# Performance work log

Measured on AMD Instinct MI355X. Metric: run time of the kernel, lower is better.

Reference implementation:

```python
import jax, jax.numpy as jnp
import numpy as np

H = 16
D_NOPE = 128
D_ROPE = 64
D_V = 128
ROPE_BASE = 10000.0
NEG = -1e9


def rotate_half(x):
    h = x.shape[-1] // 2
    return jnp.concatenate([-x[..., h:], x[..., :h]], axis=-1)


def rope_cos_sin(L, dtype=jnp.float32):
    inv_freq = 1.0 / (ROPE_BASE ** (jnp.arange(0, D_ROPE, 2, dtype=jnp.float32) / D_ROPE))
    t = jnp.arange(L, dtype=jnp.float32)
    freqs = jnp.outer(t, inv_freq)                      # (L, D_ROPE/2)
    emb = jnp.concatenate([freqs, freqs], axis=-1)      # (L, D_ROPE)
    return jnp.cos(emb)[None, None].astype(dtype), jnp.sin(emb)[None, None].astype(dtype)


def setup_inputs() -> dict:
    key = jax.random.key(0)
    ks = jax.random.split(key, 8)
    B, L, D = 1, 2048, 2048
    dq, dc = 1536, 512
    dqk = D_NOPE + D_ROPE
    s = 0.02
    hidden_states = jax.random.normal(ks[0], (B, L, D), jnp.float32)
    # causal additive mask, shape (B,1,L,L)
    causal = jnp.tril(jnp.ones((L, L), jnp.bool_))
    attention_mask = jnp.where(causal, 0.0, NEG).astype(jnp.float32)[None, None]
    return {
        "hidden_states": hidden_states,
        "attention_mask": attention_mask,
        "Wq_down": jax.random.normal(ks[1], (D, dq), jnp.float32) * s,
        "Wq_up": jax.random.normal(ks[2], (dq, H * dqk), jnp.float32) * s,
        "Wkv_down": jax.random.normal(ks[3], (D, dc), jnp.float32) * s,
        "Wk_up": jax.random.normal(ks[4], (dc, H * dqk), jnp.float32) * s,
        "Wv_up": jax.random.normal(ks[5], (dc, H * D_V), jnp.float32) * s,
        "Wo": jax.random.normal(ks[6], (H * D_V, D), jnp.float32) * s,
    }


def reference(hidden_states, attention_mask, Wq_down, Wq_up, Wkv_down, Wk_up, Wv_up, Wo):
    B, L, D = hidden_states.shape
    dqk = D_NOPE + D_ROPE
    scale = 1.0 / np.sqrt(dqk).astype(np.float32)

    # low-rank Q path
    q = (hidden_states @ Wq_down) @ Wq_up                       # (B,L,H*dqk)
    q = q.reshape(B, L, H, dqk).transpose(0, 2, 1, 3)           # (B,H,L,dqk)
    # low-rank KV path
    c_kv = hidden_states @ Wkv_down                             # (B,L,dc)
    k = (c_kv @ Wk_up).reshape(B, L, H, dqk).transpose(0, 2, 1, 3)
    v = (c_kv @ Wv_up).reshape(B, L, H, D_V).transpose(0, 2, 1, 3)

    q_nope, q_rope = q[..., :D_NOPE], q[..., D_NOPE:]
    k_nope, k_rope = k[..., :D_NOPE], k[..., D_NOPE:]
    cos, sin = rope_cos_sin(L, hidden_states.dtype)
    q_rope = q_rope * cos + rotate_half(q_rope) * sin
    k_rope = k_rope * cos + rotate_half(k_rope) * sin
    q = jnp.concatenate([q_nope, q_rope], axis=-1)
    k = jnp.concatenate([k_nope, k_rope], axis=-1)

    scores = jnp.einsum("bhqd,bhkd->bhqk", q, k) * scale + attention_mask
    weights = jax.nn.softmax(scores.astype(jnp.float32), axis=-1).astype(q.dtype)
    attn = jnp.einsum("bhqk,bhkd->bhqd", weights, v)            # (B,H,L,D_V)
    attn = attn.transpose(0, 2, 1, 3).reshape(B, L, H * D_V)
    return attn @ Wo
```

## Files before the change

kernel.cpp:

```cpp
#include <hip/hip_runtime.h>
#include <hip/hip_bf16.h>

using bf16 = __hip_bfloat16;
typedef __bf16 bf16x8v __attribute__((ext_vector_type(8)));
typedef float f32x4 __attribute__((ext_vector_type(4)));

static constexpr int SEQ = 2048;
static constexpr int DMODEL = 2048;
static constexpr int NHEADS = 16;
static constexpr int DQKC = 192;
static constexpr int DVC = 128;
static constexpr int DQC = 1536;
static constexpr int DCC = 512;
static constexpr int HQK = NHEADS * DQKC;
static constexpr int HV = NHEADS * DVC;
static constexpr int NKV = HQK + HV;
static constexpr int NDOWN = DQC + DCC;

typedef __attribute__((address_space(1))) const void* gas_ptr;
typedef __attribute__((address_space(3))) void* las_ptr;

__device__ __forceinline__ void g2l16(const void* g, void* l) {
  __builtin_amdgcn_global_load_lds((gas_ptr)g, (las_ptr)l, 16, 0, 0);
}

__global__ __launch_bounds__(256) void gemm_bt(
    const bf16* __restrict__ A, int lda, long strideAz,
    const bf16* __restrict__ Bt, int ldb, long strideBz,
    void* __restrict__ Cv, int ldc, long strideCz,
    int K, float alpha, int c_fp32, int causal)
{
  if (causal == 1 && blockIdx.x > blockIdx.y) return;
  int Keff = K;
  if (causal == 2) Keff = min(K, ((int)blockIdx.y + 1) * 128);
  __shared__ __align__(16) bf16 As[128 * 32];
  __shared__ __align__(16) bf16 Bs[128 * 32];
  const int z = blockIdx.z;
  A += (long)z * strideAz;
  Bt += (long)z * strideBz;
  const int tid = threadIdx.x;
  const int wv = tid >> 6;
  const int lane = tid & 63;
  const int wm = (wv >> 1) * 64, wn = (wv & 1) * 64;
  const long tm = (long)blockIdx.y * 128, tn = (long)blockIdx.x * 128;
  const int r16 = lane >> 2;
  const int c8 = (lane & 3) * 8;
  const bf16* Ag = A + (tm + wv * 32 + r16) * lda + c8;
  const bf16* Bg = Bt + (tn + wv * 32 + r16) * ldb + c8;
  bf16* lA0 = &As[(wv * 32) * 32];
  bf16* lA1 = &As[(wv * 32 + 16) * 32];
  bf16* lB0 = &Bs[(wv * 32) * 32];
  bf16* lB1 = &Bs[(wv * 32 + 16) * 32];
  const int m0 = lane & 15;
  const int q8 = (lane >> 4) * 8;
  f32x4 acc[4][4] = {};
  for (int bk = 0; bk < Keff; bk += 32) {
    g2l16(Ag + bk, lA0);
    g2l16(Ag + bk + 16 * (long)lda, lA1);
    g2l16(Bg + bk, lB0);
    g2l16(Bg + bk + 16 * (long)ldb, lB1);
    __syncthreads();
    bf16x8v af[4], bfv[4];
#pragma unroll
    for (int i = 0; i < 4; i++)
      af[i] = *reinterpret_cast<const bf16x8v*>(&As[(wm + i * 16 + m0) * 32 + q8]);
#pragma unroll
    for (int i = 0; i < 4; i++)
      bfv[i] = *reinterpret_cast<const bf16x8v*>(&Bs[(wn + i * 16 + m0) * 32 + q8]);
#pragma unroll
    for (int mi = 0; mi < 4; mi++)
#pragma unroll
      for (int ni = 0; ni < 4; ni++)
        acc[mi][ni] = __builtin_amdgcn_mfma_f32_16x16x32_bf16(af[mi], bfv[ni], acc[mi][ni], 0, 0, 0);
    __syncthreads();
  }
  const int q4 = (lane >> 4) * 4;
  float* Cf = (float*)Cv;
  bf16* Cb = (bf16*)Cv;
  const long zc = (long)z * strideCz;
#pragma unroll
  for (int mi = 0; mi < 4; mi++) {
#pragma unroll
    for (int r = 0; r < 4; r++) {
      const long row = tm + wm + mi * 16 + q4 + r;
#pragma unroll
      for (int ni = 0; ni < 4; ni++) {
        const long idx = zc + row * ldc + tn + wn + ni * 16 + m0;
        const float v = acc[mi][ni][r] * alpha;
        if (c_fp32) Cf[idx] = v;
        else Cb[idx] = __float2bfloat16(v);
      }
    }
  }
}

__global__ __launch_bounds__(256) void flash_attn(
    const bf16* __restrict__ qf,
    const bf16* __restrict__ kvf,
    const bf16* __restrict__ vT,
    bf16* __restrict__ attn)
{
  __shared__ __align__(16) char smem[81920];
  const int fid = blockIdx.x;
  const int half = fid >> 8;
  const int r8 = fid & 255;
  const int h = r8 & 15;
  const int t8 = r8 >> 4;
  const int tile = half ? (31 - t8) : t8;
  const int nkt = (tile >> 1) + 1;
  const int tid = threadIdx.x;
  const int w = tid >> 6, lane = tid & 63;
  const int m0 = lane & 15, quad = lane >> 4;
  const int prow = w * 16 + m0;
  const long qrow = (long)tile * 64 + prow;

  bf16x8v qfr[6];
#pragma unroll
  for (int s = 0; s < 6; s++)
    qfr[s] = *reinterpret_cast<const bf16x8v*>(
        &qf[qrow * HQK + h * DQKC + s * 32 + quad * 8]);

  f32x4 O[8] = {};
  float mrow = -1e30f, lrow = 0.f;

  for (int kt = 0; kt < nkt; ++kt) {
    const int key0 = kt * 128;
#pragma unroll
    for (int i = 0; i < 12; i++) {
      const int u = i * 256 + tid;
      const int key = u / 24;
      const int fg = (u - key * 24) ^ (key & 7);
      g2l16(kvf + (long)(key0 + key) * NKV + h * DQKC + fg * 8, smem + u * 16);
    }
#pragma unroll
    for (int i = 0; i < 8; i++) {
      const int u = i * 256 + tid;
      const int dv = u >> 4;
      const int kg = (u & 15) ^ (dv & 15);
      g2l16(vT + (long)(h * DVC + dv) * SEQ + key0 + kg * 8, smem + 49152 + u * 16);
    }
    __syncthreads();

    f32x4 S[8] = {};
#pragma unroll
    for (int s = 0; s < 6; s++) {
#pragma unroll
      for (int mi = 0; mi < 8; mi++) {
        const int kl = mi * 16 + m0;
        const int idx = kl * 24 + ((s * 4 + quad) ^ (m0 & 7));
        const bf16x8v kb = *reinterpret_cast<const bf16x8v*>(smem + idx * 16);
        S[mi] = __builtin_amdgcn_mfma_f32_16x16x32_bf16(kb, qfr[s], S[mi], 0, 0, 0);
      }
    }
    if (kt == nkt - 1) {
#pragma unroll
      for (int mi = 0; mi < 8; mi++)
#pragma unroll
        for (int r = 0; r < 4; r++)
          if (key0 + mi * 16 + quad * 4 + r > qrow) S[mi][r] = -1e30f;
    }

    float fm = -1e30f;
#pragma unroll
    for (int mi = 0; mi < 8; mi++)
#pragma unroll
      for (int r = 0; r < 4; r++) fm = fmaxf(fm, S[mi][r]);
    fm = fmaxf(fm, __shfl_xor(fm, 16, 64));
    fm = fmaxf(fm, __shfl_xor(fm, 32, 64));
    const float newm = fmaxf(mrow, fm);
    const float alph = __expf(mrow - newm);
    mrow = newm;
    float ps = 0.f;
#pragma unroll
    for (int mi = 0; mi < 8; mi++)
#pragma unroll
      for (int r = 0; r < 4; r++) {
        const float p = __expf(S[mi][r] - newm);
        S[mi][r] = p;
        ps += p;
      }
    ps += __shfl_xor(ps, 16, 64);
    ps += __shfl_xor(ps, 32, 64);
    lrow = lrow * alph + ps;

    __syncthreads();

#pragma unroll
    for (int mi = 0; mi < 8; mi++) {
      const int k8 = mi * 2 + (quad >> 1);
      const int idx = prow * 16 + (k8 ^ (m0 & 15));
      union { unsigned int u[2]; } pk;
      unsigned short b[4];
#pragma unroll
      for (int r = 0; r < 4; r++) {
        const bf16 t = __float2bfloat16(S[mi][r]);
        b[r] = *reinterpret_cast<const unsigned short*>(&t);
      }
      pk.u[0] = (unsigned)b[0] | ((unsigned)b[1] << 16);
      pk.u[1] = (unsigned)b[2] | ((unsigned)b[3] << 16);
      *reinterpret_cast<uint2*>(smem + idx * 16 + (quad & 1) * 8) =
          make_uint2(pk.u[0], pk.u[1]);
    }
    float aO[4];
#pragma unroll
    for (int r = 0; r < 4; r++) aO[r] = __shfl(alph, quad * 4 + r, 16);
#pragma unroll
    for (int ni = 0; ni < 8; ni++)
#pragma unroll
      for (int r = 0; r < 4; r++) O[ni][r] *= aO[r];

#pragma unroll
    for (int ks = 0; ks < 4; ks++) {
      const int idxp = prow * 16 + ((ks * 4 + quad) ^ (m0 & 15));
      const bf16x8v pa = *reinterpret_cast<const bf16x8v*>(smem + idxp * 16);
#pragma unroll
      for (int ni = 0; ni < 8; ni++) {
        const int dv = ni * 16 + m0;
        const int idxv = dv * 16 + ((ks * 4 + quad) ^ (dv & 15));
        const bf16x8v vb = *reinterpret_cast<const bf16x8v*>(smem + 49152 + idxv * 16);
        O[ni] = __builtin_amdgcn_mfma_f32_16x16x32_bf16(pa, vb, O[ni], 0, 0, 0);
      }
    }
    __syncthreads();
  }

  float lO[4];
#pragma unroll
  for (int r = 0; r < 4; r++) lO[r] = 1.f / __shfl(lrow, quad * 4 + r, 16);
#pragma unroll
  for (int ni = 0; ni < 8; ni++)
#pragma unroll
    for (int r = 0; r < 4; r++)
      attn[((long)tile * 64 + w * 16 + quad * 4 + r) * HV + h * DVC + ni * 16 + m0] =
          __float2bfloat16(O[ni][r] * lO[r]);
}

__device__ __forceinline__ float tofl(float x) { return x; }
__device__ __forceinline__ float tofl(bf16 x) { return __bfloat162float(x); }

template <typename TIN>
__global__ __launch_bounds__(256) void transpose_cast(const TIN* __restrict__ in,
                                                      bf16* __restrict__ out,
                                                      int inStride, int outStride) {
  __shared__ float t[32][33];
  const int bx = blockIdx.x * 32, by = blockIdx.y * 32;
  const int tx = threadIdx.x, ty = threadIdx.y;
#pragma unroll
  for (int j = 0; j < 32; j += 8)
    t[ty + j][tx] = tofl(in[(long)(by + ty + j) * inStride + bx + tx]);
  __syncthreads();
#pragma unroll
  for (int j = 0; j < 32; j += 8)
    out[(long)(bx + ty + j) * outStride + by + tx] = __float2bfloat16(t[tx][ty + j]);
}

__global__ __launch_bounds__(256) void cast_f32_bf16(const float* __restrict__ in,
                                                     bf16* __restrict__ out, int n4) {
  int i = blockIdx.x * 256 + threadIdx.x;
  if (i < n4) {
    const float4 v = ((const float4*)in)[i];
    out[i * 4 + 0] = __float2bfloat16(v.x);
    out[i * 4 + 1] = __float2bfloat16(v.y);
    out[i * 4 + 2] = __float2bfloat16(v.z);
    out[i * 4 + 3] = __float2bfloat16(v.w);
  }
}

__global__ __launch_bounds__(256) void rope_qk(bf16* __restrict__ q, bf16* __restrict__ k) {
  const int idx = blockIdx.x * 256 + threadIdx.x;
  const int i = idx & 31;
  const int h = (idx >> 5) & 15;
  const int l = idx >> 9;
  const float inv = powf(10000.f, -(float)i * (1.f / 32.f));
  float s, c;
  sincosf((float)l * inv, &s, &c);
  const long qb = (long)l * HQK + h * DQKC + 128;
  const long kb = (long)l * NKV + h * DQKC + 128;
  {
    float x0 = __bfloat162float(q[qb + i]);
    float x1 = __bfloat162float(q[qb + i + 32]);
    q[qb + i] = __float2bfloat16(x0 * c - x1 * s);
    q[qb + i + 32] = __float2bfloat16(x1 * c + x0 * s);
  }
  {
    float x0 = __bfloat162float(k[kb + i]);
    float x1 = __bfloat162float(k[kb + i + 32]);
    k[kb + i] = __float2bfloat16(x0 * c - x1 * s);
    k[kb + i + 32] = __float2bfloat16(x1 * c + x0 * s);
  }
}

extern "C" void kernel_launch(void* const* d_in, const int* in_sizes, int n_in,
                              void* d_out, int out_size, void* d_ws, size_t ws_size,
                              hipStream_t stream) {
  const float* hs      = (const float*)d_in[0];
  const float* Wq_down = (const float*)d_in[2];
  const float* Wq_up   = (const float*)d_in[3];
  const float* Wkv_down= (const float*)d_in[4];
  const float* Wk_up   = (const float*)d_in[5];
  const float* Wv_up   = (const float*)d_in[6];
  const float* Wo      = (const float*)d_in[7];

  char* p = (char*)d_ws;
  auto alloc = [&](long elems) {
    bf16* r = (bf16*)p;
    p += ((elems * 2 + 255) / 256) * 256;
    return r;
  };
  bf16* hsb   = alloc((long)SEQ * DMODEL);
  bf16* W1T   = alloc((long)NDOWN * DMODEL);
  bf16* WquT  = alloc((long)HQK * DQC);
  bf16* WkvuT = alloc((long)NKV * DCC);
  bf16* WoT   = alloc((long)DMODEL * HV);
  bf16* qdc   = alloc((long)SEQ * NDOWN);
  bf16* qf    = alloc((long)SEQ * HQK);
  bf16* kvf   = alloc((long)SEQ * NKV);
  bf16* vT    = alloc((long)HV * SEQ);
  bf16* attn  = alloc((long)SEQ * HV);

  const float scale = 0.07216878364870323f;

  const dim3 b256(256);
  const dim3 tb(32, 8);
  cast_f32_bf16<<<dim3(SEQ * DMODEL / 4 / 256), b256, 0, stream>>>(hs, hsb, SEQ * DMODEL / 4);
  transpose_cast<float><<<dim3(DQC / 32, DMODEL / 32), tb, 0, stream>>>(Wq_down, W1T, DQC, DMODEL);
  transpose_cast<float><<<dim3(DCC / 32, DMODEL / 32), tb, 0, stream>>>(Wkv_down, W1T + (long)DQC * DMODEL, DCC, DMODEL);
  transpose_cast<float><<<dim3(HQK / 32, DQC / 32), tb, 0, stream>>>(Wq_up, WquT, HQK, DQC);
  transpose_cast<float><<<dim3(HQK / 32, DCC / 32), tb, 0, stream>>>(Wk_up, WkvuT, HQK, DCC);
  transpose_cast<float><<<dim3(HV / 32, DCC / 32), tb, 0, stream>>>(Wv_up, WkvuT + (long)HQK * DCC, HV, DCC);
  transpose_cast<float><<<dim3(DMODEL / 32, HV / 32), tb, 0, stream>>>(Wo, WoT, DMODEL, HV);

  gemm_bt<<<dim3(NDOWN / 128, SEQ / 128), b256, 0, stream>>>(
      hsb, DMODEL, 0, W1T, DMODEL, 0, qdc, NDOWN, 0, DMODEL, 1.f, 0, 0);
  gemm_bt<<<dim3(HQK / 128, SEQ / 128), b256, 0, stream>>>(
      qdc, NDOWN, 0, WquT, DQC, 0, qf, HQK, 0, DQC, scale, 0, 0);
  gemm_bt<<<dim3(NKV / 128, SEQ / 128), b256, 0, stream>>>(
      qdc + DQC, NDOWN, 0, WkvuT, DCC, 0, kvf, NKV, 0, DCC, 1.f, 0, 0);

  rope_qk<<<dim3(SEQ * NHEADS * 32 / 256), b256, 0, stream>>>(qf, kvf);
  transpose_cast<bf16><<<dim3(HV / 32, SEQ / 32), tb, 0, stream>>>(kvf + HQK, vT, NKV, SEQ);

  flash_attn<<<dim3(512), b256, 0, stream>>>(qf, kvf, vT, attn);

  gemm_bt<<<dim3(DMODEL / 128, SEQ / 128), b256, 0, stream>>>(
      attn, HV, 0, WoT, HV, 0, d_out, DMODEL, 0, HV, 1.f, 1, 0);
}
```

Baseline: 383.2 us.

## Batch weight transposes, use 64x128 GEMM tiles, fuse up-projections, shrink attention key tile

The six weight transpose-casts become one kernel launch. The GEMMs switch from 128x128 to 64x128 block tiles to launch more blocks, and the Q and KV up-projections are merged into a single dual-GEMM launch. The flash attention key tile drops from 128 to 96 keys, so less work is spent on masked keys at the causal boundary and shared memory use falls. In exchange, each GEMM block reuses less data per tile and attention runs more loop iterations with more frequent masking checks.

```diff
diff --git a/kernel.cpp b/kernel.cpp
--- a/kernel.cpp
+++ b/kernel.cpp
@@ -24,74 +24,89 @@
   __builtin_amdgcn_global_load_lds((gas_ptr)g, (las_ptr)l, 16, 0, 0);
 }
 
-__global__ __launch_bounds__(256) void gemm_bt(
-    const bf16* __restrict__ A, int lda, long strideAz,
-    const bf16* __restrict__ Bt, int ldb, long strideBz,
-    void* __restrict__ Cv, int ldc, long strideCz,
-    int K, float alpha, int c_fp32, int causal)
+template <int BM, int BN>
+__device__ __forceinline__ void gemm_core(
+    const bf16* __restrict__ A, int lda,
+    const bf16* __restrict__ Bt, int ldb,
+    void* __restrict__ Cv, int ldc,
+    int K, float alpha, int c_fp32, long tm, long tn, char* smem)
 {
-  if (causal == 1 && blockIdx.x > blockIdx.y) return;
-  int Keff = K;
-  if (causal == 2) Keff = min(K, ((int)blockIdx.y + 1) * 128);
-  __shared__ __align__(16) bf16 As[128 * 32];
-  __shared__ __align__(16) bf16 Bs[128 * 32];
-  const int z = blockIdx.z;
-  A += (long)z * strideAz;
-  Bt += (long)z * strideBz;
+  constexpr int FM = BM / 32, FN = BN / 32;
+  bf16* As = (bf16*)smem;
+  char* Bsm = smem + BM * 64;
+  bf16* Bs = (bf16*)Bsm;
   const int tid = threadIdx.x;
-  const int wv = tid >> 6;
-  const int lane = tid & 63;
-  const int wm = (wv >> 1) * 64, wn = (wv & 1) * 64;
-  const long tm = (long)blockIdx.y * 128, tn = (long)blockIdx.x * 128;
-  const int r16 = lane >> 2;
-  const int c8 = (lane & 3) * 8;
-  const bf16* Ag = A + (tm + wv * 32 + r16) * lda + c8;
-  const bf16* Bg = Bt + (tn + wv * 32 + r16) * ldb + c8;
-  bf16* lA0 = &As[(wv * 32) * 32];
-  bf16* lA1 = &As[(wv * 32 + 16) * 32];
-  bf16* lB0 = &Bs[(wv * 32) * 32];
-  bf16* lB1 = &Bs[(wv * 32 + 16) * 32];
-  const int m0 = lane & 15;
-  const int q8 = (lane >> 4) * 8;
-  f32x4 acc[4][4] = {};
-  for (int bk = 0; bk < Keff; bk += 32) {
-    g2l16(Ag + bk, lA0);
-    g2l16(Ag + bk + 16 * (long)lda, lA1);
-    g2l16(Bg + bk, lB0);
-    g2l16(Bg + bk + 16 * (long)ldb, lB1);
-    __syncthreads();
-    bf16x8v af[4], bfv[4];
-#pragma unroll
-    for (int i = 0; i < 4; i++)
+  const int w = tid >> 6, lane = tid & 63;
+  const int wm = (w >> 1) * (BM / 2), wn = (w & 1) * (BN / 2);
+  const int m0 = lane & 15, q8 = (lane >> 4) * 8;
+  f32x4 acc[FM][FN] = {};
+  for (int bk = 0; bk < K; bk += 32) {
+#pragma unroll
+    for (int i = 0; i < BM / 64; i++) {
+      const int u = i * 256 + tid;
+      g2l16(A + (tm + (u >> 2)) * (long)lda + bk + (u & 3) * 8, smem + u * 16);
+    }
+#pragma unroll
+    for (int i = 0; i < BN / 64; i++) {
+      const int u = i * 256 + tid;
+      g2l16(Bt + (tn + (u >> 2)) * (long)ldb + bk + (u & 3) * 8, Bsm + u * 16);
+    }
+    __syncthreads();
+    bf16x8v af[FM], bfv[FN];
+#pragma unroll
+    for (int i = 0; i < FM; i++)
       af[i] = *reinterpret_cast<const bf16x8v*>(&As[(wm + i * 16 + m0) * 32 + q8]);
 #pragma unroll
-    for (int i = 0; i < 4; i++)
+    for (int i = 0; i < FN; i++)
       bfv[i] = *reinterpret_cast<const bf16x8v*>(&Bs[(wn + i * 16 + m0) * 32 + q8]);
 #pragma unroll
-    for (int mi = 0; mi < 4; mi++)
-#pragma unroll
-      for (int ni = 0; ni < 4; ni++)
+    for (int mi = 0; mi < FM; mi++)
+#pragma unroll
+      for (int ni = 0; ni < FN; ni++)
         acc[mi][ni] = __builtin_amdgcn_mfma_f32_16x16x32_bf16(af[mi], bfv[ni], acc[mi][ni], 0, 0, 0);
     __syncthreads();
   }
   const int q4 = (lane >> 4) * 4;
   float* Cf = (float*)Cv;
   bf16* Cb = (bf16*)Cv;
-  const long zc = (long)z * strideCz;
-#pragma unroll
-  for (int mi = 0; mi < 4; mi++) {
+#pragma unroll
+  for (int mi = 0; mi < FM; mi++) {
 #pragma unroll
     for (int r = 0; r < 4; r++) {
       const long row = tm + wm + mi * 16 + q4 + r;
 #pragma unroll
-      for (int ni = 0; ni < 4; ni++) {
-        const long idx = zc + row * ldc + tn + wn + ni * 16 + m0;
+      for (int ni = 0; ni < FN; ni++) {
+        const long idx = row * ldc + tn + wn + ni * 16 + m0;
         const float v = acc[mi][ni][r] * alpha;
         if (c_fp32) Cf[idx] = v;
         else Cb[idx] = __float2bfloat16(v);
       }
     }
   }
+}
+
+__global__ __launch_bounds__(256) void gemm64(
+    const bf16* __restrict__ A, int lda, const bf16* __restrict__ Bt, int ldb,
+    void* __restrict__ Cv, int ldc, int K, float alpha, int c_fp32)
+{
+  __shared__ __align__(16) char smem[(64 + 128) * 64];
+  gemm_core<64, 128>(A, lda, Bt, ldb, Cv, ldc, K, alpha, c_fp32,
+                     (long)blockIdx.y * 64, (long)blockIdx.x * 128, smem);
+}
+
+__global__ __launch_bounds__(256) void gemm_dual(
+    const bf16* __restrict__ A1, int lda1, const bf16* __restrict__ B1, int ldb1,
+    void* __restrict__ C1, int ldc1, int K1, float alpha1, int nx1,
+    const bf16* __restrict__ A2, int lda2, const bf16* __restrict__ B2, int ldb2,
+    void* __restrict__ C2, int ldc2, int K2)
+{
+  __shared__ __align__(16) char smem[(64 + 128) * 64];
+  if ((int)blockIdx.x < nx1)
+    gemm_core<64, 128>(A1, lda1, B1, ldb1, C1, ldc1, K1, alpha1, 0,
+                       (long)blockIdx.y * 64, (long)blockIdx.x * 128, smem);
+  else
+    gemm_core<64, 128>(A2, lda2, B2, ldb2, C2, ldc2, K2, 1.f, 0,
+                       (long)blockIdx.y * 64, (long)((int)blockIdx.x - nx1) * 128, smem);
 }
 
 __global__ __launch_bounds__(256) void flash_attn(
@@ -100,14 +115,14 @@
     const bf16* __restrict__ vT,
     bf16* __restrict__ attn)
 {
-  __shared__ __align__(16) char smem[81920];
+  __shared__ __align__(16) char smem[69632];
   const int fid = blockIdx.x;
   const int half = fid >> 8;
   const int r8 = fid & 255;
   const int h = r8 & 15;
   const int t8 = r8 >> 4;
   const int tile = half ? (31 - t8) : t8;
-  const int nkt = (tile >> 1) + 1;
+  const int nkt = (tile * 64 + 63) / 96 + 1;
   const int tid = threadIdx.x;
   const int w = tid >> 6, lane = tid & 63;
   const int m0 = lane & 15, quad = lane >> 4;
@@ -124,9 +139,9 @@
   float mrow = -1e30f, lrow = 0.f;
 
   for (int kt = 0; kt < nkt; ++kt) {
-    const int key0 = kt * 128;
-#pragma unroll
-    for (int i = 0; i < 12; i++) {
+    const int key0 = kt * 96;
+#pragma unroll
+    for (int i = 0; i < 9; i++) {
       const int u = i * 256 + tid;
       const int key = u / 24;
       const int fg = (u - key * 24) ^ (key & 7);
@@ -137,24 +152,24 @@
       const int u = i * 256 + tid;
       const int dv = u >> 4;
       const int kg = (u & 15) ^ (dv & 15);
-      g2l16(vT + (long)(h * DVC + dv) * SEQ + key0 + kg * 8, smem + 49152 + u * 16);
-    }
-    __syncthreads();
-
-    f32x4 S[8] = {};
+      g2l16(vT + (long)(h * DVC + dv) * SEQ + key0 + kg * 8, smem + 36864 + u * 16);
+    }
+    __syncthreads();
+
+    f32x4 S[6] = {};
 #pragma unroll
     for (int s = 0; s < 6; s++) {
 #pragma unroll
-      for (int mi = 0; mi < 8; mi++) {
+      for (int mi = 0; mi < 6; mi++) {
         const int kl = mi * 16 + m0;
         const int idx = kl * 24 + ((s * 4 + quad) ^ (m0 & 7));
         const bf16x8v kb = *reinterpret_cast<const bf16x8v*>(smem + idx * 16);
         S[mi] = __builtin_amdgcn_mfma_f32_16x16x32_bf16(kb, qfr[s], S[mi], 0, 0, 0);
       }
     }
-    if (kt == nkt - 1) {
-#pragma unroll
-      for (int mi = 0; mi < 8; mi++)
+    if (key0 + 95 > tile * 64) {
+#pragma unroll
+      for (int mi = 0; mi < 6; mi++)
 #pragma unroll
         for (int r = 0; r < 4; r++)
           if (key0 + mi * 16 + quad * 4 + r > qrow) S[mi][r] = -1e30f;
@@ -162,7 +177,7 @@
 
     float fm = -1e30f;
 #pragma unroll
-    for (int mi = 0; mi < 8; mi++)
+    for (int mi = 0; mi < 6; mi++)
 #pragma unroll
       for (int r = 0; r < 4; r++) fm = fmaxf(fm, S[mi][r]);
     fm = fmaxf(fm, __shfl_xor(fm, 16, 64));
@@ -172,7 +187,7 @@
     mrow = newm;
     float ps = 0.f;
 #pragma unroll
-    for (int mi = 0; mi < 8; mi++)
+    for (int mi = 0; mi < 6; mi++)
 #pragma unroll
       for (int r = 0; r < 4; r++) {
         const float p = __expf(S[mi][r] - newm);
@@ -186,20 +201,18 @@
     __syncthreads();
 
 #pragma unroll
-    for (int mi = 0; mi < 8; mi++) {
+    for (int mi = 0; mi < 6; mi++) {
       const int k8 = mi * 2 + (quad >> 1);
       const int idx = prow * 16 + (k8 ^ (m0 & 15));
-      union { unsigned int u[2]; } pk;
       unsigned short b[4];
 #pragma unroll
       for (int r = 0; r < 4; r++) {
         const bf16 t = __float2bfloat16(S[mi][r]);
         b[r] = *reinterpret_cast<const unsigned short*>(&t);
       }
-      pk.u[0] = (unsigned)b[0] | ((unsigned)b[1] << 16);
-      pk.u[1] = (unsigned)b[2] | ((unsigned)b[3] << 16);
       *reinterpret_cast<uint2*>(smem + idx * 16 + (quad & 1) * 8) =
-          make_uint2(pk.u[0], pk.u[1]);
+          make_uint2((unsigned)b[0] | ((unsigned)b[1] << 16),
+                     (unsigned)b[2] | ((unsigned)b[3] << 16));
     }
     float aO[4];
 #pragma unroll
@@ -210,14 +223,14 @@
       for (int r = 0; r < 4; r++) O[ni][r] *= aO[r];
 
 #pragma unroll
-    for (int ks = 0; ks < 4; ks++) {
+    for (int ks = 0; ks < 3; ks++) {
       const int idxp = prow * 16 + ((ks * 4 + quad) ^ (m0 & 15));
       const bf16x8v pa = *reinterpret_cast<const bf16x8v*>(smem + idxp * 16);
 #pragma unroll
       for (int ni = 0; ni < 8; ni++) {
         const int dv = ni * 16 + m0;
         const int idxv = dv * 16 + ((ks * 4 + quad) ^ (dv & 15));
-        const bf16x8v vb = *reinterpret_cast<const bf16x8v*>(smem + 49152 + idxv * 16);
+        const bf16x8v vb = *reinterpret_cast<const bf16x8v*>(smem + 36864 + idxv * 16);
         O[ni] = __builtin_amdgcn_mfma_f32_16x16x32_bf16(pa, vb, O[ni], 0, 0, 0);
       }
     }
@@ -252,6 +265,34 @@
 #pragma unroll
   for (int j = 0; j < 32; j += 8)
     out[(long)(bx + ty + j) * outStride + by + tx] = __float2bfloat16(t[tx][ty + j]);
+}
+
+struct TPar { const float* src; bf16* dst; int C; int R; int gw; int nblk; };
+
+__global__ __launch_bounds__(256) void transpose6(TPar a, TPar b, TPar c,
+                                                  TPar d, TPar e, TPar f) {
+  int blk = blockIdx.x;
+  TPar p;
+  if (blk < a.nblk) p = a;
+  else { blk -= a.nblk;
+  if (blk < b.nblk) p = b;
+  else { blk -= b.nblk;
+  if (blk < c.nblk) p = c;
+  else { blk -= c.nblk;
+  if (blk < d.nblk) p = d;
+  else { blk -= d.nblk;
+  if (blk < e.nblk) p = e;
+  else { blk -= e.nblk; p = f; } } } } }
+  const int bx = (blk % p.gw) * 32, by = (blk / p.gw) * 32;
+  __shared__ float t[32][33];
+  const int tx = threadIdx.x, ty = threadIdx.y;
+#pragma unroll
+  for (int j = 0; j < 32; j += 8)
+    t[ty + j][tx] = p.src[(long)(by + ty + j) * p.C + bx + tx];
+  __syncthreads();
+#pragma unroll
+  for (int j = 0; j < 32; j += 8)
+    p.dst[(long)(bx + ty + j) * p.R + by + tx] = __float2bfloat16(t[tx][ty + j]);
 }
 
 __global__ __launch_bounds__(256) void cast_f32_bf16(const float* __restrict__ in,
@@ -323,25 +364,28 @@
   const dim3 b256(256);
   const dim3 tb(32, 8);
   cast_f32_bf16<<<dim3(SEQ * DMODEL / 4 / 256), b256, 0, stream>>>(hs, hsb, SEQ * DMODEL / 4);
-  transpose_cast<float><<<dim3(DQC / 32, DMODEL / 32), tb, 0, stream>>>(Wq_down, W1T, DQC, DMODEL);
-  transpose_cast<float><<<dim3(DCC / 32, DMODEL / 32), tb, 0, stream>>>(Wkv_down, W1T + (long)DQC * DMODEL, DCC, DMODEL);
-  transpose_cast<float><<<dim3(HQK / 32, DQC / 32), tb, 0, stream>>>(Wq_up, WquT, HQK, DQC);
-  transpose_cast<float><<<dim3(HQK / 32, DCC / 32), tb, 0, stream>>>(Wk_up, WkvuT, HQK, DCC);
-  transpose_cast<float><<<dim3(HV / 32, DCC / 32), tb, 0, stream>>>(Wv_up, WkvuT + (long)HQK * DCC, HV, DCC);
-  transpose_cast<float><<<dim3(DMODEL / 32, HV / 32), tb, 0, stream>>>(Wo, WoT, DMODEL, HV);
-
-  gemm_bt<<<dim3(NDOWN / 128, SEQ / 128), b256, 0, stream>>>(
-      hsb, DMODEL, 0, W1T, DMODEL, 0, qdc, NDOWN, 0, DMODEL, 1.f, 0, 0);
-  gemm_bt<<<dim3(HQK / 128, SEQ / 128), b256, 0, stream>>>(
-      qdc, NDOWN, 0, WquT, DQC, 0, qf, HQK, 0, DQC, scale, 0, 0);
-  gemm_bt<<<dim3(NKV / 128, SEQ / 128), b256, 0, stream>>>(
-      qdc + DQC, NDOWN, 0, WkvuT, DCC, 0, kvf, NKV, 0, DCC, 1.f, 0, 0);
+
+  TPar ta{Wq_down,  W1T,                      DQC,    DMODEL, DQC / 32,    (DQC / 32) * (DMODEL / 32)};
+  TPar tb2{Wkv_down, W1T + (long)DQC * DMODEL, DCC,    DMODEL, DCC / 32,    (DCC / 32) * (DMODEL / 32)};
+  TPar tc{Wq_up,    WquT,                     HQK,    DQC,    HQK / 32,    (HQK / 32) * (DQC / 32)};
+  TPar td{Wk_up,    WkvuT,                    HQK,    DCC,    HQK / 32,    (HQK / 32) * (DCC / 32)};
+  TPar te{Wv_up,    WkvuT + (long)HQK * DCC,  HV,     DCC,    HV / 32,     (HV / 32) * (DCC / 32)};
+  TPar tf{Wo,       WoT,                      DMODEL, HV,     DMODEL / 32, (DMODEL / 32) * (HV / 32)};
+  const int tblk = ta.nblk + tb2.nblk + tc.nblk + td.nblk + te.nblk + tf.nblk;
+  transpose6<<<dim3(tblk), tb, 0, stream>>>(ta, tb2, tc, td, te, tf);
+
+  gemm64<<<dim3(NDOWN / 128, SEQ / 64), b256, 0, stream>>>(
+      hsb, DMODEL, W1T, DMODEL, qdc, NDOWN, DMODEL, 1.f, 0);
+
+  gemm_dual<<<dim3(HQK / 128 + NKV / 128, SEQ / 64), b256, 0, stream>>>(
+      qdc, NDOWN, WquT, DQC, qf, HQK, DQC, scale, HQK / 128,
+      qdc + DQC, NDOWN, WkvuT, DCC, kvf, NKV, DCC);
 
   rope_qk<<<dim3(SEQ * NHEADS * 32 / 256), b256, 0, stream>>>(qf, kvf);
   transpose_cast<bf16><<<dim3(HV / 32, SEQ / 32), tb, 0, stream>>>(kvf + HQK, vT, NKV, SEQ);
 
   flash_attn<<<dim3(512), b256, 0, stream>>>(qf, kvf, vT, attn);
 
-  gemm_bt<<<dim3(DMODEL / 128, SEQ / 128), b256, 0, stream>>>(
-      attn, HV, 0, WoT, HV, 0, d_out, DMODEL, 0, HV, 1.f, 1, 0);
-}
+  gemm64<<<dim3(DMODEL / 128, SEQ / 64), b256, 0, stream>>>(
+      attn, HV, WoT, HV, d_out, DMODEL, HV, 1.f, 1);
+}
```

Result: faster. 341.1 us (-11.0%).
